# Performance work log

Measured on AMD Instinct MI355X. Metric: run time of the kernel, lower is better.

Reference implementation:

```python
import jax, jax.numpy as jnp
import numpy as np

WINDOW = 5  # window_size from init


def _avg_pool3d(x, k):
    # Matches F.avg_pool3d(kernel=k, stride=1, padding=k//2,
    # count_include_pad=True): windowed sum with zero padding / k^3.
    pad = k // 2
    s = jax.lax.reduce_window(
        x, 0.0, jax.lax.add,
        window_dimensions=(1, 1, k, k, k),
        window_strides=(1, 1, 1, 1, 1),
        padding=[(0, 0), (0, 0), (pad, pad), (pad, pad), (pad, pad)],
    )
    return s / float(k ** 3)


def setup_inputs() -> dict:
    key = jax.random.key(0)
    k1, k2 = jax.random.split(key)
    shape = (2, 1, 160, 192, 192)  # [B, C, D, H, W]
    source = jax.random.normal(k1, shape, dtype=jnp.float32)
    target = jax.random.normal(k2, shape, dtype=jnp.float32)
    return {"source": source, "target": target}


def reference(source, target):
    conv = lambda x: _avg_pool3d(x, WINDOW)
    src_mean = conv(source)
    tgt_mean = conv(target)
    src_var = conv(source * source) - src_mean * src_mean
    tgt_var = conv(target * target) - tgt_mean * tgt_mean
    cross = conv(source * target) - src_mean * tgt_mean
    lncc = cross * cross / (src_var * tgt_var + 1e-5)
    loss = 1.0 - jnp.mean(lncc)
    return jnp.nan_to_num(loss, nan=1.0, posinf=1.0, neginf=1.0)
```

## Files before the change

### kernel.cpp

```cpp
#include <hip/hip_runtime.h>
#include <math.h>

#define W_ 192
#define H_ 192
#define D_ 160
#define B_ 2
#define CHUNK 40
#define TILE 16
#define HALO 20
#define NTOT 11796480.0f

struct Q { float ss, tt, s2, t2, st; };

__global__ __launch_bounds__(256) void lncc_main(const float* __restrict__ src,
                                                 const float* __restrict__ tgt,
                                                 float* __restrict__ acc) {
    __shared__ float2 tileP[HALO][HALO];
    __shared__ float  wsum[4];

    const int tx  = threadIdx.x, ty = threadIdx.y;
    const int tid = ty * TILE + tx;
    const int bz  = blockIdx.z;
    const int b   = bz >> 2;
    const int z0  = (bz & 3) * CHUNK;
    const int bx0 = blockIdx.x * TILE - 2;
    const int by0 = blockIdx.y * TILE - 2;

    Q r0 = {}, r1 = {}, r2 = {}, r3 = {}, r4 = {};
    float lsum = 0.0f;

    for (int zp = z0 - 2; zp < z0 + CHUNK + 2; ++zp) {
        Q cur = {};
        if (zp >= 0 && zp < D_) {
            __syncthreads();
            const size_t planeBase = (size_t)(b * D_ + zp) * (size_t)(H_ * W_);
            for (int f = tid; f < HALO * HALO; f += TILE * TILE) {
                int r  = f / HALO;
                int c  = f - r * HALO;
                int gy = by0 + r, gx = bx0 + c;
                float sv = 0.0f, tv = 0.0f;
                if (gx >= 0 && gx < W_ && gy >= 0 && gy < H_) {
                    size_t idx = planeBase + (size_t)gy * W_ + (size_t)gx;
                    sv = src[idx];
                    tv = tgt[idx];
                }
                tileP[r][c] = make_float2(sv, tv);
            }
            __syncthreads();
            #pragma unroll
            for (int dy = 0; dy < 5; ++dy) {
                #pragma unroll
                for (int dx = 0; dx < 5; ++dx) {
                    float2 v = tileP[ty + dy][tx + dx];
                    cur.ss += v.x;
                    cur.tt += v.y;
                    cur.s2 = fmaf(v.x, v.x, cur.s2);
                    cur.t2 = fmaf(v.y, v.y, cur.t2);
                    cur.st = fmaf(v.x, v.y, cur.st);
                }
            }
        }
        r0 = r1; r1 = r2; r2 = r3; r3 = r4; r4 = cur;

        if (zp >= z0 + 2) {
            const float inv = 1.0f / 125.0f;
            float ssum  = r0.ss + r1.ss + r2.ss + r3.ss + r4.ss;
            float tsum  = r0.tt + r1.tt + r2.tt + r3.tt + r4.tt;
            float s2sum = r0.s2 + r1.s2 + r2.s2 + r3.s2 + r4.s2;
            float t2sum = r0.t2 + r1.t2 + r2.t2 + r3.t2 + r4.t2;
            float stsum = r0.st + r1.st + r2.st + r3.st + r4.st;
            float ms = ssum * inv, mt = tsum * inv;
            float vs = s2sum * inv - ms * ms;
            float vt = t2sum * inv - mt * mt;
            float cr = stsum * inv - ms * mt;
            lsum += cr * cr / (vs * vt + 1e-5f);
        }
    }

    #pragma unroll
    for (int off = 32; off > 0; off >>= 1)
        lsum += __shfl_down(lsum, off, 64);
    if ((tid & 63) == 0) wsum[tid >> 6] = lsum;
    __syncthreads();
    if (tid == 0) {
        float t = wsum[0] + wsum[1] + wsum[2] + wsum[3];
        atomicAdd(acc, t);
    }
}

__global__ void lncc_zero(float* acc) { *acc = 0.0f; }

__global__ void lncc_finalize(const float* __restrict__ acc, float* __restrict__ out) {
    float loss = 1.0f - (*acc) * (1.0f / NTOT);
    if (isnan(loss) || isinf(loss)) loss = 1.0f;
    *out = loss;
}

extern "C" void kernel_launch(void* const* d_in, const int* in_sizes, int n_in,
                              void* d_out, int out_size, void* d_ws, size_t ws_size,
                              hipStream_t stream) {
    const float* src = (const float*)d_in[0];
    const float* tgt = (const float*)d_in[1];
    float* out = (float*)d_out;
    float* acc = (float*)d_ws;

    lncc_zero<<<dim3(1), dim3(1), 0, stream>>>(acc);

    dim3 grid(W_ / TILE, H_ / TILE, B_ * (D_ / CHUNK));
    dim3 block(TILE, TILE, 1);
    lncc_main<<<grid, block, 0, stream>>>(src, tgt, acc);

    lncc_finalize<<<dim3(1), dim3(1), 0, stream>>>(acc, out);
}
```

Before: 183.6 us.

## Make the LNCC box filter separable with shared row sums and a running z-sum

Splits the 5x5 in-plane window sum into two passes. A horizontal pass writes per-row partial sums of the five moments to shared memory, and a vertical pass adds five of those rows per thread. The z-direction sum becomes a running total that adds the new plane and subtracts the oldest one from a ring. The z chunk is halved to double the block count, launch bounds request higher occupancy, the plane loop is fully unrolled, and the division is replaced by a hardware reciprocal. This cuts LDS reads and ALU work per voxel. In exchange it reloads more halo planes per block, and the running-sum subtraction plus the approximate reciprocal can introduce small float drift.

```diff
diff --git a/kernel.cpp b/kernel.cpp
--- a/kernel.cpp
+++ b/kernel.cpp
@@ -5,75 +5,108 @@
 #define H_ 192
 #define D_ 160
 #define B_ 2
-#define CHUNK 40
 #define TILE 16
 #define HALO 20
+#define CHUNK 20
+#define PLANES (CHUNK + 4)
 #define NTOT 11796480.0f
 
 struct Q { float ss, tt, s2, t2, st; };
 
-__global__ __launch_bounds__(256) void lncc_main(const float* __restrict__ src,
-                                                 const float* __restrict__ tgt,
-                                                 float* __restrict__ acc) {
-    __shared__ float2 tileP[HALO][HALO];
+__global__ __launch_bounds__(256, 8) void lncc_main(const float* __restrict__ src,
+                                                    const float* __restrict__ tgt,
+                                                    float* __restrict__ acc) {
+    __shared__ float2 raw[HALO][HALO + 1];
+    __shared__ float4 rs4[HALO][TILE + 1];
+    __shared__ float  rs1[HALO][TILE + 1];
     __shared__ float  wsum[4];
 
     const int tx  = threadIdx.x, ty = threadIdx.y;
     const int tid = ty * TILE + tx;
     const int bz  = blockIdx.z;
-    const int b   = bz >> 2;
-    const int z0  = (bz & 3) * CHUNK;
+    const int b   = bz >> 3;
+    const int z0  = (bz & 7) * CHUNK;
     const int bx0 = blockIdx.x * TILE - 2;
     const int by0 = blockIdx.y * TILE - 2;
 
-    Q r0 = {}, r1 = {}, r2 = {}, r3 = {}, r4 = {};
+    Q ring[5] = {{0,0,0,0,0},{0,0,0,0,0},{0,0,0,0,0},{0,0,0,0,0},{0,0,0,0,0}};
+    Q zs = {0,0,0,0,0};
     float lsum = 0.0f;
 
-    for (int zp = z0 - 2; zp < z0 + CHUNK + 2; ++zp) {
-        Q cur = {};
+    #pragma unroll
+    for (int i = 0; i < PLANES; ++i) {
+        const int zp = z0 - 2 + i;
+        Q ys = {0,0,0,0,0};
         if (zp >= 0 && zp < D_) {
+            const size_t planeBase = (size_t)(b * D_ + zp) * (size_t)(H_ * W_);
+            {
+                int f = tid;
+                #pragma unroll
+                for (int rep = 0; rep < 2; ++rep, f += 256) {
+                    if (f < HALO * HALO) {
+                        int r  = f / HALO;
+                        int c  = f - r * HALO;
+                        int gy = by0 + r, gx = bx0 + c;
+                        float sv = 0.0f, tv = 0.0f;
+                        if ((unsigned)gx < (unsigned)W_ && (unsigned)gy < (unsigned)H_) {
+                            size_t idx = planeBase + (size_t)gy * W_ + (size_t)gx;
+                            sv = src[idx];
+                            tv = tgt[idx];
+                        }
+                        raw[r][c] = make_float2(sv, tv);
+                    }
+                }
+            }
             __syncthreads();
-            const size_t planeBase = (size_t)(b * D_ + zp) * (size_t)(H_ * W_);
-            for (int f = tid; f < HALO * HALO; f += TILE * TILE) {
-                int r  = f / HALO;
-                int c  = f - r * HALO;
-                int gy = by0 + r, gx = bx0 + c;
-                float sv = 0.0f, tv = 0.0f;
-                if (gx >= 0 && gx < W_ && gy >= 0 && gy < H_) {
-                    size_t idx = planeBase + (size_t)gy * W_ + (size_t)gx;
-                    sv = src[idx];
-                    tv = tgt[idx];
+            {
+                int p = tid;
+                #pragma unroll
+                for (int rep = 0; rep < 2; ++rep, p += 256) {
+                    if (p < HALO * TILE) {
+                        int ry = p >> 4, rx = p & 15;
+                        float a0 = 0, a1 = 0, a2 = 0, a3 = 0, a4 = 0;
+                        #pragma unroll
+                        for (int dx = 0; dx < 5; ++dx) {
+                            float2 v = raw[ry][rx + dx];
+                            a0 += v.x;
+                            a1 += v.y;
+                            a2 = fmaf(v.x, v.x, a2);
+                            a3 = fmaf(v.y, v.y, a3);
+                            a4 = fmaf(v.x, v.y, a4);
+                        }
+                        rs4[ry][rx] = make_float4(a0, a1, a2, a3);
+                        rs1[ry][rx] = a4;
+                    }
                 }
-                tileP[r][c] = make_float2(sv, tv);
             }
             __syncthreads();
             #pragma unroll
             for (int dy = 0; dy < 5; ++dy) {
-                #pragma unroll
-                for (int dx = 0; dx < 5; ++dx) {
-                    float2 v = tileP[ty + dy][tx + dx];
-                    cur.ss += v.x;
-                    cur.tt += v.y;
-                    cur.s2 = fmaf(v.x, v.x, cur.s2);
-                    cur.t2 = fmaf(v.y, v.y, cur.t2);
-                    cur.st = fmaf(v.x, v.y, cur.st);
-                }
+                float4 a = rs4[ty + dy][tx];
+                float  g = rs1[ty + dy][tx];
+                ys.ss += a.x;
+                ys.tt += a.y;
+                ys.s2 += a.z;
+                ys.t2 += a.w;
+                ys.st += g;
             }
         }
-        r0 = r1; r1 = r2; r2 = r3; r3 = r4; r4 = cur;
+        const int slot = i % 5;
+        zs.ss += ys.ss - ring[slot].ss;
+        zs.tt += ys.tt - ring[slot].tt;
+        zs.s2 += ys.s2 - ring[slot].s2;
+        zs.t2 += ys.t2 - ring[slot].t2;
+        zs.st += ys.st - ring[slot].st;
+        ring[slot] = ys;
 
-        if (zp >= z0 + 2) {
+        if (i >= 4) {
             const float inv = 1.0f / 125.0f;
-            float ssum  = r0.ss + r1.ss + r2.ss + r3.ss + r4.ss;
-            float tsum  = r0.tt + r1.tt + r2.tt + r3.tt + r4.tt;
-            float s2sum = r0.s2 + r1.s2 + r2.s2 + r3.s2 + r4.s2;
-            float t2sum = r0.t2 + r1.t2 + r2.t2 + r3.t2 + r4.t2;
-            float stsum = r0.st + r1.st + r2.st + r3.st + r4.st;
-            float ms = ssum * inv, mt = tsum * inv;
-            float vs = s2sum * inv - ms * ms;
-            float vt = t2sum * inv - mt * mt;
-            float cr = stsum * inv - ms * mt;
-            lsum += cr * cr / (vs * vt + 1e-5f);
+            float ms = zs.ss * inv, mt = zs.tt * inv;
+            float vs = fmaf(-ms, ms, zs.s2 * inv);
+            float vt = fmaf(-mt, mt, zs.t2 * inv);
+            float cr = fmaf(-ms, mt, zs.st * inv);
+            float den = fmaf(vs, vt, 1e-5f);
+            lsum = fmaf(cr * cr, __builtin_amdgcn_rcpf(den), lsum);
         }
     }
 
```

Result: slower. 344.0 us (+87.4%).
